# Optimization experiments

Hardware: AMD Instinct MI355X
Metric: run time of the kernel (lower is better)

## Reference

```python
import jax, jax.numpy as jnp
import numpy as np

H = 10   # GRU hidden size
L = 10   # num layers
E = 400  # embedding dim
V = 100000
T, B = 84, 96


def gru_layer(x, w_ih, w_hh, b_ih, b_hh, reverse):
    # x: (T, B, in_dim); w_ih: (3H, in_dim); w_hh: (3H, H)
    xp = jnp.einsum('tbi,gi->tbg', x, w_ih) + b_ih  # (T, B, 3H)
    if reverse:
        xp = xp[::-1]

    def step(h, xt):
        gh = h @ w_hh.T + b_hh
        xr, xz, xn = jnp.split(xt, 3, axis=-1)
        hr, hz, hn = jnp.split(gh, 3, axis=-1)
        r = jax.nn.sigmoid(xr + hr)
        z = jax.nn.sigmoid(xz + hz)
        n = jnp.tanh(xn + r * hn)
        h_new = (1.0 - z) * n + z * h
        return h_new, h_new

    h0 = jnp.zeros((x.shape[1], H), x.dtype)
    _, ys = jax.lax.scan(step, h0, xp)
    if reverse:
        ys = ys[::-1]
    return ys  # (T, B, H)


def setup_inputs():
    key = jax.random.key(0)
    ks = jax.random.split(key, 12)
    s = 0.05
    return {
        'x': jax.random.randint(ks[0], (T, B), 0, V),
        'emb': jax.random.normal(ks[1], (V, E), jnp.float32) * 0.1,
        'w_ih0': jax.random.normal(ks[2], (2, 3 * H, E), jnp.float32) * s,
        'w_hh0': jax.random.normal(ks[3], (2, 3 * H, H), jnp.float32) * s,
        'b_ih0': jax.random.normal(ks[4], (2, 3 * H), jnp.float32) * s,
        'b_hh0': jax.random.normal(ks[5], (2, 3 * H), jnp.float32) * s,
        'w_ih': jax.random.normal(ks[6], (L - 1, 2, 3 * H, 2 * H), jnp.float32) * s,
        'w_hh': jax.random.normal(ks[7], (L - 1, 2, 3 * H, H), jnp.float32) * s,
        'b_ih': jax.random.normal(ks[8], (L - 1, 2, 3 * H), jnp.float32) * s,
        'b_hh': jax.random.normal(ks[9], (L - 1, 2, 3 * H), jnp.float32) * s,
        'lin_w': jax.random.normal(ks[10], (19, 336), jnp.float32) * s,
        'lin_b': jax.random.normal(ks[11], (19,), jnp.float32) * s,
    }


def reference(x, emb, w_ih0, w_hh0, b_ih0, b_hh0, w_ih, w_hh, b_ih, b_hh, lin_w, lin_b):
    out = emb[x]  # (T, B, 400)
    for l in range(L):
        if l == 0:
            wi, wh, bi, bh = w_ih0, w_hh0, b_ih0, b_hh0
        else:
            wi, wh, bi, bh = w_ih[l - 1], w_hh[l - 1], b_ih[l - 1], b_hh[l - 1]
        fwd = gru_layer(out, wi[0], wh[0], bi[0], bh[0], False)
        bwd = gru_layer(out, wi[1], wh[1], bi[1], bh[1], True)
        out = jnp.concatenate([fwd, bwd], axis=-1)  # (T, B, 20)
        # dropout p=0.2 between layers is disabled (eval-mode reference)
    # AvgPool2d(3)/MaxPool2d(3) on 3D input pool over (batch, feature) dims
    trimmed = out[:, : (B // 3) * 3, :18].reshape(T, B // 3, 3, 6, 3)
    avg = trimmed.mean(axis=(2, 4))  # (T, B//3, 6)
    mx = trimmed.max(axis=(2, 4))    # (T, B//3, 6)
    cat = jnp.concatenate([avg, mx], axis=2)  # (T, B//3, 12)
    flat = cat.reshape(-1, 336)  # (96, 336)
    # dropout p=0.2 disabled (eval-mode reference)
    return jax.nn.sigmoid(flat @ lin_w.T + lin_b)
```

## Files before the change

kernel.cpp:

```cpp
#include <hip/hip_runtime.h>
#include <math.h>

#define TT 84
#define BB 96
#define GB 6
#define NG 16
#define NTOK (TT*BB)
#define RW4 6

#define S_RZ (-1.4426950408889634f)
#define S_N  (-2.8853900817779268f)

typedef float v2f __attribute__((ext_vector_type(2)));
typedef float v4f __attribute__((ext_vector_type(4)));

__device__ __forceinline__ float frcp(float x)  { return __builtin_amdgcn_rcpf(x); }
__device__ __forceinline__ float fexp2(float x) { return __builtin_amdgcn_exp2f(x); }
__device__ __forceinline__ v2f   fma2(v2f a, v2f b, v2f c) {
    return __builtin_elementwise_fma(a, b, c);
}

__global__ __launch_bounds__(256) void proj0_kernel(
    const int* __restrict__ x, const float* __restrict__ emb,
    const float* __restrict__ wih0, const float* __restrict__ bih0,
    float* __restrict__ xp, unsigned int* __restrict__ bar)
{
    if (blockIdx.x == 0 && threadIdx.x == 0) bar[0] = 0u;
    __shared__ float4 xrow[32][100];
    const int tok0 = blockIdx.x * 32;
    for (int u = threadIdx.x; u < 32*100; u += 256) {
        int tk = u / 100, i4 = u % 100;
        int row = x[tok0 + tk];
        xrow[tk][i4] = ((const float4*)emb)[row*100 + i4];
    }
    __syncthreads();
    const int g64 = threadIdx.x & 63;
    const int q   = threadIdx.x >> 6;
    if (g64 >= 60) return;
    const int dir = g64 / 30, gg = g64 % 30;
    const float sc = (gg < 20) ? S_RZ : S_N;
    const float bias = bih0[dir*30 + gg];
    const int ch  = (gg < 20) ? (gg % 10) : (gg - 20);
    const int idx = (gg < 20) ? (ch*2 + gg/10) : (20 + ch);
    float acc[8];
    #pragma unroll
    for (int c = 0; c < 8; ++c) acc[c] = bias;
    const float4* w4 = ((const float4*)wih0) + (dir*30 + gg)*100;
    for (int i4 = 0; i4 < 100; ++i4) {
        float4 w = w4[i4];
        #pragma unroll
        for (int c = 0; c < 8; ++c) {
            float4 xv = xrow[q*8 + c][i4];
            acc[c] += w.x*xv.x + w.y*xv.y + w.z*xv.z + w.w*xv.w;
        }
    }
    #pragma unroll
    for (int c = 0; c < 8; ++c) {
        int tok = tok0 + q*8 + c;
        int t = tok / BB, b = tok % BB;
        xp[((size_t)((dir*TT + t)*BB + b))*30 + idx] = acc[c]*sc;
    }
}

__device__ __forceinline__ void proj20(
    const float4* A, const float* wpr, const float* wpz, const float* wpn,
    float bir, float biz, float bin, float& xr, float& xz, float& xn)
{
    float a[24];
    #pragma unroll
    for (int q = 0; q < 6; ++q) {
        a[4*q]=A[q].x; a[4*q+1]=A[q].y; a[4*q+2]=A[q].z; a[4*q+3]=A[q].w;
    }
    xr = bir; xz = biz; xn = bin;
    #pragma unroll
    for (int c = 0; c < 20; ++c) {
        float av = a[c + (c >= 10 ? 2 : 0)];
        xr = fmaf(wpr[c], av, xr); xz = fmaf(wpz[c], av, xz); xn = fmaf(wpn[c], av, xn);
    }
}

template<bool LAST>
__device__ __forceinline__ void scan_layer(
    const float* __restrict__ xb,
    const float* __restrict__ wh, const float* __restrict__ bh3,
    float* __restrict__ actF, float* __restrict__ actG,
    int bl, int j, bool act_ln, int b, int dir, int dt, int t0)
{
    v2f wr2[5], wz2[5], wn2[5];
    {
        const v2f* p0 = (const v2f*)(wh + j*10);
        const v2f* p1 = (const v2f*)(wh + (10+j)*10);
        const v2f* p2 = (const v2f*)(wh + (20+j)*10);
        #pragma unroll
        for (int q = 0; q < 5; ++q) {
            wr2[q] = p0[q] * S_RZ;
            wz2[q] = p1[q] * S_RZ;
            wn2[q] = p2[q] * S_N;
        }
    }
    const v2f br2 = {bh3[j]*S_RZ,    0.f};
    const v2f bz2 = {bh3[10+j]*S_RZ, 0.f};
    const v2f bn2 = {bh3[20+j]*S_N,  0.f};

    v2f H0 = {0,0}, H1 = {0,0}, H2 = {0,0}, H3 = {0,0}, H4 = {0,0};
    float hown = 0.f;
    int t = t0;

    const int xoff = 2*j, noff = 20 + j;
    v2f  rzA = *(const v2f*)(xb + (size_t)(t0*BB + b)*30 + xoff);
    float xnA = xb[(size_t)(t0*BB + b)*30 + noff];
    v2f  rzB = *(const v2f*)(xb + (size_t)((t0+dt)*BB + b)*30 + xoff);
    float xnB = xb[(size_t)((t0+dt)*BB + b)*30 + noff];

    const float* arow = actF;

    #define GRU_STEP(RZ, XN)                                                  \
    {                                                                         \
        v2f ar = fma2(wr2[0], H0, br2);                                       \
        v2f az = fma2(wz2[0], H0, bz2);                                       \
        v2f an2 = fma2(wn2[0], H0, bn2);                                      \
        ar = fma2(wr2[1], H1, ar); az = fma2(wz2[1], H1, az); an2 = fma2(wn2[1], H1, an2); \
        ar = fma2(wr2[2], H2, ar); az = fma2(wz2[2], H2, az); an2 = fma2(wn2[2], H2, an2); \
        ar = fma2(wr2[3], H3, ar); az = fma2(wz2[3], H3, az); an2 = fma2(wn2[3], H3, an2); \
        ar = fma2(wr2[4], H4, ar); az = fma2(wz2[4], H4, az); an2 = fma2(wn2[4], H4, an2); \
        float r  = frcp(1.f + fexp2((RZ.x + ar.x) + ar.y));                   \
        float z  = frcp(1.f + fexp2((RZ.y + az.x) + az.y));                   \
        float an = fmaf(r, an2.x + an2.y, XN);                                \
        float n  = fmaf(2.f, frcp(1.f + fexp2(an)), -1.f);                    \
        float hnew = n + z*(hown - n);                                        \
        hown = hnew;                                                          \
        int rowf = (t*GB + bl)*24 + dir*12;                                   \
        ((float*)arow)[rowf + j] = hnew;                        \
        const v4f* hr = (const v4f*)(arow + rowf);                            \
        v4f ha = hr[0], hb = hr[1];                      \
        v2f hc = *(const v2f*)(arow + rowf + 8);             \
        H0 = ha.xy; H1 = ha.zw; H2 = hb.xy; H3 = hb.zw; H4 = hc;              \
        __builtin_amdgcn_sched_barrier(0);                                    \
        if (LAST) { if (act_ln) actG[(size_t)(t*BB + b)*20 + dir*10 + j] = hnew; } \
    }

    #pragma unroll 1
    for (int s = 0; s < TT; s += 2) {
        GRU_STEP(rzA, xnA)
        {
            int tp = t + 2*dt; tp = tp < 0 ? 0 : (tp > TT-1 ? TT-1 : tp);
            const float* px = xb + (size_t)(tp*BB + b)*30;
            rzA = *(const v2f*)(px + xoff); xnA = px[noff];
            t += dt;
        }
        GRU_STEP(rzB, xnB)
        {
            int tp = t + 2*dt; tp = tp < 0 ? 0 : (tp > TT-1 ? TT-1 : tp);
            const float* px = xb + (size_t)(tp*BB + b)*30;
            rzB = *(const v2f*)(px + xoff); xnB = px[noff];
            t += dt;
        }
    }
    #undef GRU_STEP
}

__global__ __launch_bounds__(256, 1) void mega_kernel(
    float* __restrict__ xp,
    const float* __restrict__ whh0, const float* __restrict__ bhh0,
    const float* __restrict__ wih,  const float* __restrict__ bih,
    const float* __restrict__ whh,  const float* __restrict__ bhh,
    const float* __restrict__ lin_w, const float* __restrict__ lin_b,
    float* __restrict__ actG, unsigned int* __restrict__ bar,
    float* __restrict__ out)
{
    __shared__ float4 act4[TT*GB*RW4];

    const int tid  = threadIdx.x;
    const int grp  = blockIdx.x;

    const int dir  = (tid >> 6) & 1;
    const int lane = tid & 63;
    int bl = lane / 10; if (bl > 5) bl = 5;
    int j  = lane - bl*10; if (j > 9) j = 9;
    const bool act_ln = (lane < 60);
    const int b  = grp*GB + bl;
    const int dt = dir ? -1 : 1;
    const int t0 = dir ? TT-1 : 0;

    const int half = tid / 120;
    const int prr  = tid % 120;
    const int dp   = prr / 60;
    const int prr2 = prr % 60;
    const int blp  = prr2 / 10;
    const int jp   = prr2 % 10;

    #pragma unroll 1
    for (int l = 0; l < 9; ++l) {
        if (tid < 128) {
            const float* wh  = (l == 0) ? (whh0 + dir*300)
                                        : (whh + (size_t)((l-1)*2 + dir)*300);
            const float* bh3 = (l == 0) ? (bhh0 + dir*30)
                                        : (bhh + (size_t)((l-1)*2 + dir)*30);
            scan_layer<false>(xp + (size_t)dir*TT*BB*30, wh, bh3,
                              (float*)act4, actG, bl, j, act_ln, b, dir, dt, t0);
        }
        __syncthreads();
        if (tid < 240) {
            const float* wi = wih + (size_t)(l*2 + dp)*600;
            const float* bi = bih + (size_t)(l*2 + dp)*30;
            float wpr[20], wpz[20], wpn[20];
            {
                const float4* p0 = (const float4*)(wi + jp*20);
                const float4* p1 = (const float4*)(wi + (10+jp)*20);
                const float4* p2 = (const float4*)(wi + (20+jp)*20);
                #pragma unroll
                for (int q = 0; q < 5; ++q) {
                    float4 a = p0[q]; wpr[4*q]=a.x*S_RZ; wpr[4*q+1]=a.y*S_RZ; wpr[4*q+2]=a.z*S_RZ; wpr[4*q+3]=a.w*S_RZ;
                    float4 c = p1[q]; wpz[4*q]=c.x*S_RZ; wpz[4*q+1]=c.y*S_RZ; wpz[4*q+2]=c.z*S_RZ; wpz[4*q+3]=c.w*S_RZ;
                    float4 d = p2[q]; wpn[4*q]=d.x*S_N;  wpn[4*q+1]=d.y*S_N;  wpn[4*q+2]=d.z*S_N;  wpn[4*q+3]=d.w*S_N;
                }
            }
            const float bir = bi[jp]*S_RZ, biz = bi[10+jp]*S_RZ, bin = bi[20+jp]*S_N;
            const int bg = grp*GB + blp;
            #pragma unroll 1
            for (int t = half*(TT/2); t < (half+1)*(TT/2); ++t) {
                float xr, xz, xn;
                proj20(&act4[(t*GB + blp)*RW4], wpr, wpz, wpn, bir, biz, bin, xr, xz, xn);
                float* px = xp + ((size_t)(dp*TT + t)*BB + bg)*30;
                *(v2f*)(px + 2*jp) = (v2f){xr, xz};
                px[20+jp] = xn;
            }
        }
        __syncthreads();
    }
    if (tid < 128) {
        const float* wh  = whh + (size_t)(8*2 + dir)*300;
        const float* bh3 = bhh + (size_t)(8*2 + dir)*30;
        scan_layer<true>(xp + (size_t)dir*TT*BB*30, wh, bh3,
                         (float*)act4, actG, bl, j, act_ln, b, dir, dt, t0);
    }

    __threadfence();
    __syncthreads();
    if (tid == 0) {
        __hip_atomic_fetch_add(bar, 1u, __ATOMIC_ACQ_REL, __HIP_MEMORY_SCOPE_AGENT);
        while (__hip_atomic_load(bar, __ATOMIC_ACQUIRE, __HIP_MEMORY_SCOPE_AGENT) < (unsigned)NG)
            __builtin_amdgcn_s_sleep(1);
    }
    __syncthreads();
    __threadfence();

    float* feat = (float*)act4;
    for (int u = tid; u < GB*336; u += 256) {
        int q = u / 336, v = u % 336;
        int r = grp*GB + q;
        int qq = v / 12, f = v % 12;
        int pair = r*28 + qq;
        int t = pair / 32, bb = pair % 32;
        int jj = (f < 6) ? f : f - 6;
        float acc = (f < 6) ? 0.f : -1e30f;
        #pragma unroll
        for (int i = 0; i < 3; ++i) {
            #pragma unroll
            for (int kk = 0; kk < 3; ++kk) {
                float vv = actG[(size_t)(t*BB + bb*3 + i)*20 + jj*3 + kk];
                if (f < 6) acc += vv; else acc = fmaxf(acc, vv);
            }
        }
        feat[u] = (f < 6) ? acc*(1.f/9.f) : acc;
    }
    __syncthreads();
    if (tid < GB*19) {
        int q = tid / 19, o = tid % 19;
        int r = grp*GB + q;
        float acc = lin_b[o];
        const float* wrow = lin_w + o*336;
        const float* frow = feat + q*336;
        for (int v = 0; v < 336; ++v) acc = fmaf(frow[v], wrow[v], acc);
        out[r*19 + o] = frcp(1.f + __expf(-acc));
    }
}

extern "C" void kernel_launch(void* const* d_in, const int* in_sizes, int n_in,
                              void* d_out, int out_size, void* d_ws, size_t ws_size,
                              hipStream_t stream)
{
    const int*   x     = (const int*)  d_in[0];
    const float* emb   = (const float*)d_in[1];
    const float* wih0  = (const float*)d_in[2];
    const float* whh0  = (const float*)d_in[3];
    const float* bih0  = (const float*)d_in[4];
    const float* bhh0  = (const float*)d_in[5];
    const float* wih   = (const float*)d_in[6];
    const float* whh   = (const float*)d_in[7];
    const float* bih   = (const float*)d_in[8];
    const float* bhh   = (const float*)d_in[9];
    const float* lin_w = (const float*)d_in[10];
    const float* lin_b = (const float*)d_in[11];
    float* out = (float*)d_out;

    float* xp0  = (float*)d_ws;
    float* actG = xp0 + (size_t)2*NTOK*30;
    unsigned int* bar = (unsigned int*)(actG + (size_t)NTOK*20);

    proj0_kernel<<<252, 256, 0, stream>>>(x, emb, wih0, bih0, xp0, bar);
    mega_kernel<<<NG, 256, 0, stream>>>(xp0, whh0, bhh0, wih, bih, whh, bhh,
                                        lin_w, lin_b, actG, bar, out);
}
```

Before: 438.5 us.

## Run forward and backward GRU scans in one wavefront with interleaved steps

```diff
diff --git a/kernel.cpp b/kernel.cpp
--- a/kernel.cpp
+++ b/kernel.cpp
@@ -79,84 +79,116 @@
     }
 }
 
+__device__ __forceinline__ float gru_gates(
+    v2f RZ, float XN,
+    const v2f* w5r, const v2f* w5z, const v2f* w5n,
+    v2f br2, v2f bz2, v2f bn2,
+    v2f H0, v2f H1, v2f H2, v2f H3, v2f H4, float hown)
+{
+    v2f ar  = fma2(w5r[0], H0, br2);
+    v2f az  = fma2(w5z[0], H0, bz2);
+    v2f an2 = fma2(w5n[0], H0, bn2);
+    ar = fma2(w5r[1], H1, ar); az = fma2(w5z[1], H1, az); an2 = fma2(w5n[1], H1, an2);
+    ar = fma2(w5r[2], H2, ar); az = fma2(w5z[2], H2, az); an2 = fma2(w5n[2], H2, an2);
+    ar = fma2(w5r[3], H3, ar); az = fma2(w5z[3], H3, az); an2 = fma2(w5n[3], H3, an2);
+    ar = fma2(w5r[4], H4, ar); az = fma2(w5z[4], H4, az); an2 = fma2(w5n[4], H4, an2);
+    float r  = frcp(1.f + fexp2((RZ.x + ar.x) + ar.y));
+    float z  = frcp(1.f + fexp2((RZ.y + az.x) + az.y));
+    float an = fmaf(r, an2.x + an2.y, XN);
+    float n  = fmaf(2.f, frcp(1.f + fexp2(an)), -1.f);
+    return n + z*(hown - n);
+}
+
 template<bool LAST>
-__device__ __forceinline__ void scan_layer(
-    const float* __restrict__ xb,
-    const float* __restrict__ wh, const float* __restrict__ bh3,
-    float* __restrict__ actF, float* __restrict__ actG,
-    int bl, int j, bool act_ln, int b, int dir, int dt, int t0)
-{
-    v2f wr2[5], wz2[5], wn2[5];
+__device__ __forceinline__ void scan_dual(
+    const float* __restrict__ xpF, const float* __restrict__ xpB,
+    const float* __restrict__ whF, const float* __restrict__ bhF,
+    const float* __restrict__ whB, const float* __restrict__ bhB,
+    float* __restrict__ arow, float* __restrict__ actG,
+    int bl, int j, bool act_ln, int b)
+{
+    v2f wrF[5], wzF[5], wnF[5], wrB[5], wzB[5], wnB[5];
     {
-        const v2f* p0 = (const v2f*)(wh + j*10);
-        const v2f* p1 = (const v2f*)(wh + (10+j)*10);
-        const v2f* p2 = (const v2f*)(wh + (20+j)*10);
+        const v2f* f0 = (const v2f*)(whF + j*10);
+        const v2f* f1 = (const v2f*)(whF + (10+j)*10);
+        const v2f* f2 = (const v2f*)(whF + (20+j)*10);
+        const v2f* b0 = (const v2f*)(whB + j*10);
+        const v2f* b1 = (const v2f*)(whB + (10+j)*10);
+        const v2f* b2 = (const v2f*)(whB + (20+j)*10);
         #pragma unroll
         for (int q = 0; q < 5; ++q) {
-            wr2[q] = p0[q] * S_RZ;
-            wz2[q] = p1[q] * S_RZ;
-            wn2[q] = p2[q] * S_N;
-        }
-    }
-    const v2f br2 = {bh3[j]*S_RZ,    0.f};
-    const v2f bz2 = {bh3[10+j]*S_RZ, 0.f};
-    const v2f bn2 = {bh3[20+j]*S_N,  0.f};
-
-    v2f H0 = {0,0}, H1 = {0,0}, H2 = {0,0}, H3 = {0,0}, H4 = {0,0};
-    float hown = 0.f;
-    int t = t0;
+            wrF[q] = f0[q] * S_RZ;  wzF[q] = f1[q] * S_RZ;  wnF[q] = f2[q] * S_N;
+            wrB[q] = b0[q] * S_RZ;  wzB[q] = b1[q] * S_RZ;  wnB[q] = b2[q] * S_N;
+        }
+    }
+    const v2f brF = {bhF[j]*S_RZ, 0.f}, bzF = {bhF[10+j]*S_RZ, 0.f}, bnF = {bhF[20+j]*S_N, 0.f};
+    const v2f brB = {bhB[j]*S_RZ, 0.f}, bzB = {bhB[10+j]*S_RZ, 0.f}, bnB = {bhB[20+j]*S_N, 0.f};
+
+    v2f HF0={0,0}, HF1={0,0}, HF2={0,0}, HF3={0,0}, HF4={0,0};
+    v2f HB0={0,0}, HB1={0,0}, HB2={0,0}, HB3={0,0}, HB4={0,0};
+    float hoF = 0.f, hoB = 0.f;
 
     const int xoff = 2*j, noff = 20 + j;
-    v2f  rzA = *(const v2f*)(xb + (size_t)(t0*BB + b)*30 + xoff);
-    float xnA = xb[(size_t)(t0*BB + b)*30 + noff];
-    v2f  rzB = *(const v2f*)(xb + (size_t)((t0+dt)*BB + b)*30 + xoff);
-    float xnB = xb[(size_t)((t0+dt)*BB + b)*30 + noff];
-
-    const float* arow = actF;
-
-    #define GRU_STEP(RZ, XN)                                                  \
+    v2f  rzF0 = *(const v2f*)(xpF + (size_t)(0*BB + b)*30 + xoff);
+    float xnF0 = xpF[(size_t)(0*BB + b)*30 + noff];
+    v2f  rzF1 = *(const v2f*)(xpF + (size_t)(1*BB + b)*30 + xoff);
+    float xnF1 = xpF[(size_t)(1*BB + b)*30 + noff];
+    v2f  rzB0 = *(const v2f*)(xpB + (size_t)((TT-1)*BB + b)*30 + xoff);
+    float xnB0 = xpB[(size_t)((TT-1)*BB + b)*30 + noff];
+    v2f  rzB1 = *(const v2f*)(xpB + (size_t)((TT-2)*BB + b)*30 + xoff);
+    float xnB1 = xpB[(size_t)((TT-2)*BB + b)*30 + noff];
+
+    int tF = 0, tB = TT-1;
+
+    #define DUAL_STEP(RZF, XNF, RZB, XNB)                                     \
     {                                                                         \
-        v2f ar = fma2(wr2[0], H0, br2);                                       \
-        v2f az = fma2(wz2[0], H0, bz2);                                       \
-        v2f an2 = fma2(wn2[0], H0, bn2);                                      \
-        ar = fma2(wr2[1], H1, ar); az = fma2(wz2[1], H1, az); an2 = fma2(wn2[1], H1, an2); \
-        ar = fma2(wr2[2], H2, ar); az = fma2(wz2[2], H2, az); an2 = fma2(wn2[2], H2, an2); \
-        ar = fma2(wr2[3], H3, ar); az = fma2(wz2[3], H3, az); an2 = fma2(wn2[3], H3, an2); \
-        ar = fma2(wr2[4], H4, ar); az = fma2(wz2[4], H4, az); an2 = fma2(wn2[4], H4, an2); \
-        float r  = frcp(1.f + fexp2((RZ.x + ar.x) + ar.y));                   \
-        float z  = frcp(1.f + fexp2((RZ.y + az.x) + az.y));                   \
-        float an = fmaf(r, an2.x + an2.y, XN);                                \
-        float n  = fmaf(2.f, frcp(1.f + fexp2(an)), -1.f);                    \
-        float hnew = n + z*(hown - n);                                        \
-        hown = hnew;                                                          \
-        int rowf = (t*GB + bl)*24 + dir*12;                                   \
-        ((float*)arow)[rowf + j] = hnew;                        \
-        const v4f* hr = (const v4f*)(arow + rowf);                            \
-        v4f ha = hr[0], hb = hr[1];                      \
-        v2f hc = *(const v2f*)(arow + rowf + 8);             \
-        H0 = ha.xy; H1 = ha.zw; H2 = hb.xy; H3 = hb.zw; H4 = hc;              \
+        float hnF = gru_gates(RZF, XNF, wrF, wzF, wnF, brF, bzF, bnF,         \
+                              HF0,HF1,HF2,HF3,HF4, hoF);                      \
+        float hnB = gru_gates(RZB, XNB, wrB, wzB, wnB, brB, bzB, bnB,         \
+                              HB0,HB1,HB2,HB3,HB4, hoB);                      \
+        hoF = hnF; hoB = hnB;                                                 \
+        int rowF = (tF*GB + bl)*24;                                           \
+        int rowB = (tB*GB + bl)*24 + 12;                                      \
+        arow[rowF + j] = hnF;                                   \
+        arow[rowB + j] = hnB;                                   \
+        const v4f* hrF = (const v4f*)(arow + rowF);                           \
+        v4f haF = hrF[0], hbF = hrF[1];                                       \
+        v2f hcF = *(const v2f*)(arow + rowF + 8);                             \
+        const v4f* hrB = (const v4f*)(arow + rowB);                           \
+        v4f haB = hrB[0], hbB = hrB[1];                                       \
+        v2f hcB = *(const v2f*)(arow + rowB + 8);                             \
+        HF0=haF.xy; HF1=haF.zw; HF2=hbF.xy; HF3=hbF.zw; HF4=hcF;              \
+        HB0=haB.xy; HB1=haB.zw; HB2=hbB.xy; HB3=hbB.zw; HB4=hcB;              \
         __builtin_amdgcn_sched_barrier(0);                                    \
-        if (LAST) { if (act_ln) actG[(size_t)(t*BB + b)*20 + dir*10 + j] = hnew; } \
+        if (LAST) { if (act_ln) {                                             \
+            actG[(size_t)(tF*BB + b)*20 + j]      = hnF;                      \
+            actG[(size_t)(tB*BB + b)*20 + 10 + j] = hnB; } }                  \
     }
 
     #pragma unroll 1
     for (int s = 0; s < TT; s += 2) {
-        GRU_STEP(rzA, xnA)
+        DUAL_STEP(rzF0, xnF0, rzB0, xnB0)
         {
-            int tp = t + 2*dt; tp = tp < 0 ? 0 : (tp > TT-1 ? TT-1 : tp);
-            const float* px = xb + (size_t)(tp*BB + b)*30;
-            rzA = *(const v2f*)(px + xoff); xnA = px[noff];
-            t += dt;
-        }
-        GRU_STEP(rzB, xnB)
+            int tpF = tF + 2; tpF = tpF > TT-1 ? TT-1 : tpF;
+            int tpB = tB - 2; tpB = tpB < 0 ? 0 : tpB;
+            const float* pf = xpF + (size_t)(tpF*BB + b)*30;
+            const float* pb = xpB + (size_t)(tpB*BB + b)*30;
+            rzF0 = *(const v2f*)(pf + xoff); xnF0 = pf[noff];
+            rzB0 = *(const v2f*)(pb + xoff); xnB0 = pb[noff];
+            tF += 1; tB -= 1;
+        }
+        DUAL_STEP(rzF1, xnF1, rzB1, xnB1)
         {
-            int tp = t + 2*dt; tp = tp < 0 ? 0 : (tp > TT-1 ? TT-1 : tp);
-            const float* px = xb + (size_t)(tp*BB + b)*30;
-            rzB = *(const v2f*)(px + xoff); xnB = px[noff];
-            t += dt;
-        }
-    }
-    #undef GRU_STEP
+            int tpF = tF + 2; tpF = tpF > TT-1 ? TT-1 : tpF;
+            int tpB = tB - 2; tpB = tpB < 0 ? 0 : tpB;
+            const float* pf = xpF + (size_t)(tpF*BB + b)*30;
+            const float* pb = xpB + (size_t)(tpB*BB + b)*30;
+            rzF1 = *(const v2f*)(pf + xoff); xnF1 = pf[noff];
+            rzB1 = *(const v2f*)(pb + xoff); xnB1 = pb[noff];
+            tF += 1; tB -= 1;
+        }
+    }
+    #undef DUAL_STEP
 }
 
 __global__ __launch_bounds__(256, 1) void mega_kernel(
@@ -172,15 +204,12 @@
 
     const int tid  = threadIdx.x;
     const int grp  = blockIdx.x;
-
-    const int dir  = (tid >> 6) & 1;
     const int lane = tid & 63;
+
     int bl = lane / 10; if (bl > 5) bl = 5;
     int j  = lane - bl*10; if (j > 9) j = 9;
     const bool act_ln = (lane < 60);
     const int b  = grp*GB + bl;
-    const int dt = dir ? -1 : 1;
-    const int t0 = dir ? TT-1 : 0;
 
     const int half = tid / 120;
     const int prr  = tid % 120;
@@ -189,15 +218,18 @@
     const int blp  = prr2 / 10;
     const int jp   = prr2 % 10;
 
+    float* xpF = xp;
+    float* xpB = xp + (size_t)TT*BB*30;
+
     #pragma unroll 1
     for (int l = 0; l < 9; ++l) {
-        if (tid < 128) {
-            const float* wh  = (l == 0) ? (whh0 + dir*300)
-                                        : (whh + (size_t)((l-1)*2 + dir)*300);
-            const float* bh3 = (l == 0) ? (bhh0 + dir*30)
-                                        : (bhh + (size_t)((l-1)*2 + dir)*30);
-            scan_layer<false>(xp + (size_t)dir*TT*BB*30, wh, bh3,
-                              (float*)act4, actG, bl, j, act_ln, b, dir, dt, t0);
+        if (tid < 64) {
+            const float* whF = (l == 0) ? whh0            : (whh + (size_t)((l-1)*2    )*300);
+            const float* whB = (l == 0) ? (whh0 + 300)    : (whh + (size_t)((l-1)*2 + 1)*300);
+            const float* bhF = (l == 0) ? bhh0            : (bhh + (size_t)((l-1)*2    )*30);
+            const float* bhB = (l == 0) ? (bhh0 + 30)     : (bhh + (size_t)((l-1)*2 + 1)*30);
+            scan_dual<false>(xpF, xpB, whF, bhF, whB, bhB,
+                             (float*)act4, actG, bl, j, act_ln, b);
         }
         __syncthreads();
         if (tid < 240) {
@@ -228,11 +260,11 @@
         }
         __syncthreads();
     }
-    if (tid < 128) {
-        const float* wh  = whh + (size_t)(8*2 + dir)*300;
-        const float* bh3 = bhh + (size_t)(8*2 + dir)*30;
-        scan_layer<true>(xp + (size_t)dir*TT*BB*30, wh, bh3,
-                         (float*)act4, actG, bl, j, act_ln, b, dir, dt, t0);
+    if (tid < 64) {
+        scan_dual<true>(xpF, xpB,
+                        whh + (size_t)(8*2    )*300, bhh + (size_t)(8*2    )*30,
+                        whh + (size_t)(8*2 + 1)*300, bhh + (size_t)(8*2 + 1)*30,
+                        (float*)act4, actG, bl, j, act_ln, b);
     }
 
     __threadfence();
```

After: 505.6 us. +15.3%, slower.
